# Performance work log

Measured on AMD Instinct MI355X. Metric: run time of the kernel, lower is better.

## Reference

```python
import jax, jax.numpy as jnp
import numpy as np
import math

HEAD = 4
B, N, C = 8, 1024, 256


def setup_inputs() -> dict:
    key = jax.random.key(0)
    k1, k2, k3, k4, k5 = jax.random.split(key, 5)
    query = jax.random.normal(k1, (B, N, C), dtype=jnp.float32)
    keyt = jax.random.normal(k2, (B, N, C), dtype=jnp.float32)
    value = jax.random.normal(k3, (B, N, C), dtype=jnp.float32)
    mask = jax.random.randint(k4, (B, N, N), 0, 2).astype(bool)
    dis = jax.random.normal(k5, (B, N, N), dtype=jnp.float32)
    return {"query": query, "key": keyt, "value": value, "mask": mask, "dis": dis}


def reference(query, key, value, mask, dis):
    Bq, Nq, Cq = key.shape
    d = Cq // HEAD
    # split heads: [B,N,C] -> [h,B,N,d]
    q = query.reshape(Bq, Nq, HEAD, d).transpose(2, 0, 1, 3)
    k = key.reshape(Bq, Nq, HEAD, d).transpose(2, 0, 1, 3)
    v = value.reshape(Bq, Nq, HEAD, d).transpose(2, 0, 1, 3)
    # scores: [h,B,N,N]; note: dis added BEFORE scaling, as in the torch code
    scores = jnp.einsum('hbnd,hbmd->hbnm', q, k)
    scores = scores + dis[None]            # dis broadcasts over head dim
    scores = scores / math.sqrt(d)
    scores = jnp.where(mask[None], -jnp.inf, scores)
    p_attn = jax.nn.softmax(scores, axis=-1)
    out = jnp.einsum('hbnm,hbmd->hbnd', p_attn, v)  # [h,B,N,d]
    out = out.transpose(1, 2, 0, 3).reshape(Bq, Nq, Cq)
    return out, p_attn
```

## Files before the change

### kernel.cpp

```cpp
#include <hip/hip_runtime.h>
#include <math.h>

#define HEADS 4
#define BATCH 8
#define SEQ   1024
#define CH    256
#define DH    64
#define RB    16

typedef float  floatx4  __attribute__((ext_vector_type(4)));
typedef short  shortx8  __attribute__((ext_vector_type(8)));
typedef short  shortx4  __attribute__((ext_vector_type(4)));

__device__ __forceinline__ unsigned short f2bf(float f) {
    unsigned u = __float_as_uint(f);
    unsigned r = u + 0x7FFFu + ((u >> 16) & 1u);
    return (unsigned short)(r >> 16);
}
__device__ __forceinline__ shortx8 pack8(float4 a, float4 b) {
    shortx8 r;
    r[0] = (short)f2bf(a.x); r[1] = (short)f2bf(a.y);
    r[2] = (short)f2bf(a.z); r[3] = (short)f2bf(a.w);
    r[4] = (short)f2bf(b.x); r[5] = (short)f2bf(b.y);
    r[6] = (short)f2bf(b.z); r[7] = (short)f2bf(b.w);
    return r;
}

__global__ __launch_bounds__(256)
void prep(const float* __restrict__ q, const float* __restrict__ k,
          const float* __restrict__ v, const void* __restrict__ maskp,
          unsigned short* __restrict__ qb, unsigned short* __restrict__ kb,
          unsigned short* __restrict__ vt, unsigned* __restrict__ pm)
{
    __shared__ unsigned short tl[64][68];
    const int t = threadIdx.x;
    const int bid = blockIdx.x;
    if (bid < 2048) {
        const float* src = (bid < 1024) ? q : k;
        unsigned short* dst = (bid < 1024) ? qb : kb;
        const float sc = (bid < 1024) ? 0.125f : 1.0f;
        size_t idx = (size_t)(bid & 1023) * 2048 + (size_t)t * 8;
        float4 a = *(const float4*)(src + idx);
        float4 b = *(const float4*)(src + idx + 4);
        a.x *= sc; a.y *= sc; a.z *= sc; a.w *= sc;
        b.x *= sc; b.y *= sc; b.z *= sc; b.w *= sc;
        *(shortx8*)(dst + idx) = pack8(a, b);
        return;
    }
    if (bid < 2560) {
        const int vb = bid - 2048;
        const int nt = vb & 15, h = (vb >> 4) & 3, b = vb >> 6;
        const int n0 = nt * 64;
        const float* vsrc = v + ((size_t)(b * SEQ + n0)) * CH + h * DH;
        #pragma unroll
        for (int it = 0; it < 4; ++it) {
            int fid = it * 256 + t;
            int n = fid >> 4, cc = (fid & 15) * 4;
            float4 x = *(const float4*)(vsrc + (size_t)n * CH + cc);
            tl[n][cc]     = f2bf(x.x);
            tl[n][cc + 1] = f2bf(x.y);
            tl[n][cc + 2] = f2bf(x.z);
            tl[n][cc + 3] = f2bf(x.w);
        }
        __syncthreads();
        unsigned short* vout = vt + ((size_t)((b * HEADS + h) * DH)) * SEQ + n0;
        #pragma unroll
        for (int it = 0; it < 2; ++it) {
            int cid = it * 256 + t;
            int d = cid >> 3, nc = cid & 7;
            shortx8 r;
            #pragma unroll
            for (int j = 0; j < 8; ++j) r[j] = (short)tl[nc * 8 + j][d];
            *(shortx8*)(vout + (size_t)d * SEQ + nc * 8) = r;
        }
        return;
    }
    const int vb2 = bid - 2560;
    const int b = vb2 >> 7, rg = vb2 & 127;
    const int sub = t >> 5, wq = t & 31;
    const int row = rg * 8 + sub;
    const int w_ = wq >> 2, qd_ = wq & 3;
    int fl;
    {
        const unsigned* mw = (const unsigned*)maskp;
        const int lane = t & 63;
        int found = 0;
        #pragma unroll
        for (int j = 0; j < 16; ++j)
            if (mw[lane * 16 + j] & 0xFFFFFF00u) found = 1;
        fl = (__ballot(found != 0) != 0ULL) ? 1 : 0;
    }
    const unsigned char* m8  = (const unsigned char*)maskp;
    const int*           m32 = (const int*)maskp;
    unsigned u = 0;
    #pragma unroll
    for (int mc = 0; mc < 8; ++mc) {
        #pragma unroll
        for (int r = 0; r < 4; ++r) {
            size_t idx = ((size_t)(b * SEQ + row)) * SEQ
                       + mc * 128 + w_ * 16 + qd_ * 4 + r;
            int mk = fl ? (int)m8[idx] : m32[idx];
            u |= (mk ? 1u : 0u) << (mc * 4 + r);
        }
    }
    pm[(((size_t)b * SEQ + row) << 5) + wq] = u;
}

__global__ __launch_bounds__(64)
void attn_wave(const unsigned short* __restrict__ qb,
               const unsigned short* __restrict__ kbf,
               const unsigned short* __restrict__ vt,
               const unsigned* __restrict__ pm,
               const float* __restrict__ dis, float* __restrict__ out,
               float* __restrict__ pout)
{
    __shared__ unsigned short ps[2][16][40];

    const int t   = threadIdx.x;
    const int bid = blockIdx.x;
    const int b   = bid & (BATCH - 1);
    const int h   = (bid >> 3) & (HEADS - 1);
    const int n0  = (bid >> 5) * RB;
    const int ln  = t & 15;
    const int qd  = t >> 4;

    const unsigned short* qrow = qb + ((size_t)(b * SEQ + n0 + ln)) * CH + h * DH;
    shortx8 aq0 = *(const shortx8*)(qrow + qd * 8);
    shortx8 aq1 = *(const shortx8*)(qrow + 32 + qd * 8);

    const unsigned short* kbase = kbf + ((size_t)(b * SEQ)) * CH + h * DH;
    const unsigned short* vbase = vt + ((size_t)((b * HEADS + h) * DH)) * SEQ;
    const float* disrow =
        dis + ((size_t)(b * SEQ + n0 + ln)) * SEQ + qd * 4;
    const unsigned* pmrow = pm + (((size_t)(b * SEQ + n0 + ln)) << 5) + qd;

    float sum = 0.f;
    for (int wg = 0; wg < 8; ++wg) {
        const unsigned mw = pmrow[wg * 4];
        #pragma unroll 4
        for (int mc = 0; mc < 8; ++mc) {
            const int cb = mc * 128 + wg * 16;
            const unsigned short* krow = kbase + (size_t)(cb + ln) * CH;
            shortx8 kf0 = *(const shortx8*)(krow + qd * 8);
            shortx8 kf1 = *(const shortx8*)(krow + 32 + qd * 8);
            float4 dv = *(const float4*)(disrow + cb);
            floatx4 acc = {0.f, 0.f, 0.f, 0.f};
            acc = __builtin_amdgcn_mfma_f32_16x16x32_bf16(kf0, aq0, acc, 0, 0, 0);
            acc = __builtin_amdgcn_mfma_f32_16x16x32_bf16(kf1, aq1, acc, 0, 0, 0);
            float x0 = __expf(fmaf(dv.x, 0.125f, acc[0]));
            float x1 = __expf(fmaf(dv.y, 0.125f, acc[1]));
            float x2 = __expf(fmaf(dv.z, 0.125f, acc[2]));
            float x3 = __expf(fmaf(dv.w, 0.125f, acc[3]));
            if ((mw >> (mc * 4 + 0)) & 1u) x0 = 0.f;
            if ((mw >> (mc * 4 + 1)) & 1u) x1 = 0.f;
            if ((mw >> (mc * 4 + 2)) & 1u) x2 = 0.f;
            if ((mw >> (mc * 4 + 3)) & 1u) x3 = 0.f;
            sum += x0 + x1 + x2 + x3;
        }
    }
    sum += __shfl_xor(sum, 16);
    sum += __shfl_xor(sum, 32);
    const float inv = 1.0f / sum;

    floatx4 o0 = {0.f,0.f,0.f,0.f}, o1 = {0.f,0.f,0.f,0.f};
    floatx4 o2 = {0.f,0.f,0.f,0.f}, o3 = {0.f,0.f,0.f,0.f};
    float* prow = pout + ((size_t)((h * BATCH + b) * SEQ + n0 + ln)) * SEQ
                + qd * 4;
    int par = 0;
    for (int wp = 0; wp < 4; ++wp) {
        const unsigned mw0 = pmrow[(2 * wp) * 4];
        const unsigned mw1 = pmrow[(2 * wp + 1) * 4];
        #pragma unroll 2
        for (int mc = 0; mc < 8; ++mc) {
            const int cb = mc * 128 + wp * 32;
            const unsigned short* vk = vbase + cb + qd * 8;
            shortx8 vf0 = *(const shortx8*)(vk + (size_t)(0 * 16 + ln) * SEQ);
            shortx8 vf1 = *(const shortx8*)(vk + (size_t)(1 * 16 + ln) * SEQ);
            shortx8 vf2 = *(const shortx8*)(vk + (size_t)(2 * 16 + ln) * SEQ);
            shortx8 vf3 = *(const shortx8*)(vk + (size_t)(3 * 16 + ln) * SEQ);
            const unsigned short* kr0 = kbase + (size_t)(cb + ln) * CH;
            const unsigned short* kr1 = kbase + (size_t)(cb + 16 + ln) * CH;
            shortx8 k00 = *(const shortx8*)(kr0 + qd * 8);
            shortx8 k01 = *(const shortx8*)(kr0 + 32 + qd * 8);
            shortx8 k10 = *(const shortx8*)(kr1 + qd * 8);
            shortx8 k11 = *(const shortx8*)(kr1 + 32 + qd * 8);
            float4 dv0 = *(const float4*)(disrow + cb);
            float4 dv1 = *(const float4*)(disrow + cb + 16);
            floatx4 a0 = {0.f,0.f,0.f,0.f}, a1 = {0.f,0.f,0.f,0.f};
            a0 = __builtin_amdgcn_mfma_f32_16x16x32_bf16(k00, aq0, a0, 0, 0, 0);
            a0 = __builtin_amdgcn_mfma_f32_16x16x32_bf16(k01, aq1, a0, 0, 0, 0);
            a1 = __builtin_amdgcn_mfma_f32_16x16x32_bf16(k10, aq0, a1, 0, 0, 0);
            a1 = __builtin_amdgcn_mfma_f32_16x16x32_bf16(k11, aq1, a1, 0, 0, 0);
            float p0[4], p1[4];
            #pragma unroll
            for (int r = 0; r < 4; ++r) {
                float e0 = __expf(fmaf(((const float*)&dv0)[r], 0.125f, a0[r]));
                float e1 = __expf(fmaf(((const float*)&dv1)[r], 0.125f, a1[r]));
                if ((mw0 >> (mc * 4 + r)) & 1u) e0 = 0.f;
                if ((mw1 >> (mc * 4 + r)) & 1u) e1 = 0.f;
                p0[r] = e0; p1[r] = e1;
            }
            float4 pv0 = { p0[0]*inv, p0[1]*inv, p0[2]*inv, p0[3]*inv };
            float4 pv1 = { p1[0]*inv, p1[1]*inv, p1[2]*inv, p1[3]*inv };
            *(float4*)(prow + cb)      = pv0;
            *(float4*)(prow + cb + 16) = pv1;
            shortx4 e0, e1;
            e0[0] = (short)f2bf(p0[0]); e0[1] = (short)f2bf(p0[1]);
            e0[2] = (short)f2bf(p0[2]); e0[3] = (short)f2bf(p0[3]);
            e1[0] = (short)f2bf(p1[0]); e1[1] = (short)f2bf(p1[1]);
            e1[2] = (short)f2bf(p1[2]); e1[3] = (short)f2bf(p1[3]);
            *(shortx4*)&ps[par][ln][qd * 4]      = e0;
            *(shortx4*)&ps[par][ln][16 + qd * 4] = e1;
            __syncthreads();
            shortx8 af = *(const shortx8*)&ps[par][ln][qd * 8];
            o0 = __builtin_amdgcn_mfma_f32_16x16x32_bf16(af, vf0, o0, 0, 0, 0);
            o1 = __builtin_amdgcn_mfma_f32_16x16x32_bf16(af, vf1, o1, 0, 0, 0);
            o2 = __builtin_amdgcn_mfma_f32_16x16x32_bf16(af, vf2, o2, 0, 0, 0);
            o3 = __builtin_amdgcn_mfma_f32_16x16x32_bf16(af, vf3, o3, 0, 0, 0);
            par ^= 1;
        }
    }

    const float invq0 = __shfl(inv, qd * 4 + 0);
    const float invq1 = __shfl(inv, qd * 4 + 1);
    const float invq2 = __shfl(inv, qd * 4 + 2);
    const float invq3 = __shfl(inv, qd * 4 + 3);
    #pragma unroll
    for (int dr = 0; dr < 4; ++dr) {
        const float iq = (dr == 0) ? invq0 : (dr == 1) ? invq1
                       : (dr == 2) ? invq2 : invq3;
        float* orow = out + ((size_t)(b * SEQ + n0 + qd * 4 + dr)) * CH
                    + h * DH + ln;
        orow[0]  = o0[dr] * iq;
        orow[16] = o1[dr] * iq;
        orow[32] = o2[dr] * iq;
        orow[48] = o3[dr] * iq;
    }
}

extern "C" void kernel_launch(void* const* d_in, const int* in_sizes, int n_in,
                              void* d_out, int out_size, void* d_ws, size_t ws_size,
                              hipStream_t stream) {
    const float* q    = (const float*)d_in[0];
    const float* k    = (const float*)d_in[1];
    const float* v    = (const float*)d_in[2];
    const void*  mask = d_in[3];
    const float* dis  = (const float*)d_in[4];
    float* out  = (float*)d_out;
    float* pout = out + (size_t)BATCH * SEQ * CH;

    unsigned short* qb  = (unsigned short*)d_ws;
    unsigned short* kbw = qb  + (size_t)BATCH * SEQ * CH;
    unsigned short* vtw = kbw + (size_t)BATCH * SEQ * CH;
    unsigned*       pmw = (unsigned*)(vtw + (size_t)BATCH * SEQ * CH);
    (void)ws_size;

    prep<<<3584, 256, 0, stream>>>(q, k, v, mask, qb, kbw, vtw, pmw);
    attn_wave<<<HEADS * BATCH * (SEQ / RB), 64, 0, stream>>>(
        qb, kbw, vtw, pmw, dis, out, pout);
}
```

Measured before the change: 322.1 us.

## Split fused attention into QK-exp and PV kernels via a bf16 score buffer

The single-wave fused kernel, which recomputed QK^T in two passes, is replaced by two kernels. The first computes the masked exponentials with 512-thread blocks, stores them as bf16 in a workspace buffer, and writes inverse row sums. The second reads those scores back for the P·V MFMA and writes the normalized probabilities. This removes the duplicated QK/exp work and gives each launch more waves per block. The cost is extra workspace traffic for the score matrix, and the probability output is now derived from bf16-rounded values, so it loses precision.

```diff
diff --git a/kernel.cpp b/kernel.cpp
--- a/kernel.cpp
+++ b/kernel.cpp
@@ -16,6 +16,9 @@
     unsigned u = __float_as_uint(f);
     unsigned r = u + 0x7FFFu + ((u >> 16) & 1u);
     return (unsigned short)(r >> 16);
+}
+__device__ __forceinline__ float bf2f(unsigned short h) {
+    return __uint_as_float(((unsigned)h) << 16);
 }
 __device__ __forceinline__ shortx8 pack8(float4 a, float4 b) {
     shortx8 r;
@@ -106,6 +109,141 @@
     pm[(((size_t)b * SEQ + row) << 5) + wq] = u;
 }
 
+__global__ __launch_bounds__(512)
+void qk_exp(const unsigned short* __restrict__ qb,
+            const unsigned short* __restrict__ kbf,
+            const unsigned* __restrict__ pm,
+            const float* __restrict__ dis,
+            unsigned short* __restrict__ S, float* __restrict__ invs_g)
+{
+    __shared__ float wsum[8][16];
+    const int t   = threadIdx.x;
+    const int bid = blockIdx.x;
+    const int b   = bid & (BATCH - 1);
+    const int h   = (bid >> 3) & (HEADS - 1);
+    const int n0  = (bid >> 5) * RB;
+    const int lane = t & 63;
+    const int w    = t >> 6;
+    const int ln   = lane & 15;
+    const int qd   = lane >> 4;
+
+    const unsigned short* qrow = qb + ((size_t)(b * SEQ + n0 + ln)) * CH + h * DH;
+    shortx8 aq0 = *(const shortx8*)(qrow + qd * 8);
+    shortx8 aq1 = *(const shortx8*)(qrow + 32 + qd * 8);
+
+    const unsigned short* kbase = kbf + ((size_t)(b * SEQ)) * CH + h * DH;
+    const float* disrow = dis + ((size_t)(b * SEQ + n0 + ln)) * SEQ + qd * 4;
+    const unsigned mw = pm[(((size_t)(b * SEQ + n0 + ln)) << 5) + w * 4 + qd];
+    unsigned short* srow =
+        S + ((size_t)((h * BATCH + b) * SEQ + n0 + ln)) * SEQ + qd * 4;
+
+    float sum = 0.f;
+    #pragma unroll 4
+    for (int mc = 0; mc < 8; ++mc) {
+        const int cb = mc * 128 + w * 16;
+        const unsigned short* krow = kbase + (size_t)(cb + ln) * CH;
+        shortx8 kf0 = *(const shortx8*)(krow + qd * 8);
+        shortx8 kf1 = *(const shortx8*)(krow + 32 + qd * 8);
+        float4 dv = *(const float4*)(disrow + cb);
+        floatx4 acc = {0.f, 0.f, 0.f, 0.f};
+        acc = __builtin_amdgcn_mfma_f32_16x16x32_bf16(kf0, aq0, acc, 0, 0, 0);
+        acc = __builtin_amdgcn_mfma_f32_16x16x32_bf16(kf1, aq1, acc, 0, 0, 0);
+        float x0 = __expf(fmaf(dv.x, 0.125f, acc[0]));
+        float x1 = __expf(fmaf(dv.y, 0.125f, acc[1]));
+        float x2 = __expf(fmaf(dv.z, 0.125f, acc[2]));
+        float x3 = __expf(fmaf(dv.w, 0.125f, acc[3]));
+        if ((mw >> (mc * 4 + 0)) & 1u) x0 = 0.f;
+        if ((mw >> (mc * 4 + 1)) & 1u) x1 = 0.f;
+        if ((mw >> (mc * 4 + 2)) & 1u) x2 = 0.f;
+        if ((mw >> (mc * 4 + 3)) & 1u) x3 = 0.f;
+        sum += x0 + x1 + x2 + x3;
+        shortx4 ev;
+        ev[0] = (short)f2bf(x0); ev[1] = (short)f2bf(x1);
+        ev[2] = (short)f2bf(x2); ev[3] = (short)f2bf(x3);
+        *(shortx4*)(srow + cb) = ev;
+    }
+    sum += __shfl_xor(sum, 16);
+    sum += __shfl_xor(sum, 32);
+    if (qd == 0) wsum[w][ln] = sum;
+    __syncthreads();
+    if (w == 0 && qd == 0) {
+        float tot = 0.f;
+        #pragma unroll
+        for (int j = 0; j < 8; ++j) tot += wsum[j][ln];
+        invs_g[(h * BATCH + b) * SEQ + n0 + ln] = 1.0f / tot;
+    }
+}
+
+__global__ __launch_bounds__(256)
+void pv(const unsigned short* __restrict__ S,
+        const unsigned short* __restrict__ vt,
+        const float* __restrict__ invs_g,
+        float* __restrict__ out, float* __restrict__ pout)
+{
+    const int t   = threadIdx.x;
+    const int bid = blockIdx.x;
+    const int b   = bid & (BATCH - 1);
+    const int h   = (bid >> 3) & (HEADS - 1);
+    const int n0  = (bid >> 5) * RB;
+    const int lane = t & 63;
+    const int w    = t >> 6;
+    const int ln   = lane & 15;
+    const int qd   = lane >> 4;
+    const int c    = w * 16;
+
+    const unsigned short* srow =
+        S + ((size_t)((h * BATCH + b) * SEQ + n0 + ln)) * SEQ;
+    const unsigned short* vcol =
+        vt + ((size_t)((b * HEADS + h) * DH + c + ln)) * SEQ;
+    float* prow = pout + ((size_t)((h * BATCH + b) * SEQ + n0 + ln)) * SEQ;
+    const float inv_l = invs_g[(h * BATCH + b) * SEQ + n0 + ln];
+
+    floatx4 accA = {0.f,0.f,0.f,0.f}, accB = {0.f,0.f,0.f,0.f};
+    #pragma unroll 4
+    for (int it = 0; it < 32; it += 2) {
+        const int kk0 = it * 32 + qd * 8;
+        const int kk1 = kk0 + 32;
+        shortx8 af0 = *(const shortx8*)(srow + kk0);
+        shortx8 bf0 = *(const shortx8*)(vcol + kk0);
+        shortx8 af1 = *(const shortx8*)(srow + kk1);
+        shortx8 bf1 = *(const shortx8*)(vcol + kk1);
+        accA = __builtin_amdgcn_mfma_f32_16x16x32_bf16(af0, bf0, accA, 0, 0, 0);
+        accB = __builtin_amdgcn_mfma_f32_16x16x32_bf16(af1, bf1, accB, 0, 0, 0);
+        if (w == 0) {
+            float4 pa = { bf2f((unsigned short)af0[0]) * inv_l,
+                          bf2f((unsigned short)af0[1]) * inv_l,
+                          bf2f((unsigned short)af0[2]) * inv_l,
+                          bf2f((unsigned short)af0[3]) * inv_l };
+            float4 pb = { bf2f((unsigned short)af0[4]) * inv_l,
+                          bf2f((unsigned short)af0[5]) * inv_l,
+                          bf2f((unsigned short)af0[6]) * inv_l,
+                          bf2f((unsigned short)af0[7]) * inv_l };
+            float4 pc = { bf2f((unsigned short)af1[0]) * inv_l,
+                          bf2f((unsigned short)af1[1]) * inv_l,
+                          bf2f((unsigned short)af1[2]) * inv_l,
+                          bf2f((unsigned short)af1[3]) * inv_l };
+            float4 pd = { bf2f((unsigned short)af1[4]) * inv_l,
+                          bf2f((unsigned short)af1[5]) * inv_l,
+                          bf2f((unsigned short)af1[6]) * inv_l,
+                          bf2f((unsigned short)af1[7]) * inv_l };
+            *(float4*)(prow + kk0)     = pa;
+            *(float4*)(prow + kk0 + 4) = pb;
+            *(float4*)(prow + kk1)     = pc;
+            *(float4*)(prow + kk1 + 4) = pd;
+        }
+    }
+    floatx4 acc;
+    acc[0] = accA[0] + accB[0]; acc[1] = accA[1] + accB[1];
+    acc[2] = accA[2] + accB[2]; acc[3] = accA[3] + accB[3];
+
+    const float* ivb = invs_g + (h * BATCH + b) * SEQ + n0 + qd * 4;
+    #pragma unroll
+    for (int r = 0; r < 4; ++r) {
+        out[((size_t)(b * SEQ + n0 + qd * 4 + r)) * CH + h * DH + c + ln]
+            = acc[r] * ivb[r];
+    }
+}
+
 __global__ __launch_bounds__(64)
 void attn_wave(const unsigned short* __restrict__ qb,
                const unsigned short* __restrict__ kbf,
@@ -115,7 +253,6 @@
                float* __restrict__ pout)
 {
     __shared__ unsigned short ps[2][16][40];
-
     const int t   = threadIdx.x;
     const int bid = blockIdx.x;
     const int b   = bid & (BATCH - 1);
@@ -123,17 +260,13 @@
     const int n0  = (bid >> 5) * RB;
     const int ln  = t & 15;
     const int qd  = t >> 4;
-
     const unsigned short* qrow = qb + ((size_t)(b * SEQ + n0 + ln)) * CH + h * DH;
     shortx8 aq0 = *(const shortx8*)(qrow + qd * 8);
     shortx8 aq1 = *(const shortx8*)(qrow + 32 + qd * 8);
-
     const unsigned short* kbase = kbf + ((size_t)(b * SEQ)) * CH + h * DH;
     const unsigned short* vbase = vt + ((size_t)((b * HEADS + h) * DH)) * SEQ;
-    const float* disrow =
-        dis + ((size_t)(b * SEQ + n0 + ln)) * SEQ + qd * 4;
+    const float* disrow = dis + ((size_t)(b * SEQ + n0 + ln)) * SEQ + qd * 4;
     const unsigned* pmrow = pm + (((size_t)(b * SEQ + n0 + ln)) << 5) + qd;
-
     float sum = 0.f;
     for (int wg = 0; wg < 8; ++wg) {
         const unsigned mw = pmrow[wg * 4];
@@ -161,7 +294,6 @@
     sum += __shfl_xor(sum, 16);
     sum += __shfl_xor(sum, 32);
     const float inv = 1.0f / sum;
-
     floatx4 o0 = {0.f,0.f,0.f,0.f}, o1 = {0.f,0.f,0.f,0.f};
     floatx4 o2 = {0.f,0.f,0.f,0.f}, o3 = {0.f,0.f,0.f,0.f};
     float* prow = pout + ((size_t)((h * BATCH + b) * SEQ + n0 + ln)) * SEQ
@@ -220,7 +352,6 @@
             par ^= 1;
         }
     }
-
     const float invq0 = __shfl(inv, qd * 4 + 0);
     const float invq1 = __shfl(inv, qd * 4 + 1);
     const float invq2 = __shfl(inv, qd * 4 + 2);
@@ -249,13 +380,26 @@
     float* out  = (float*)d_out;
     float* pout = out + (size_t)BATCH * SEQ * CH;
 
+    const size_t E = (size_t)BATCH * SEQ * CH;
     unsigned short* qb  = (unsigned short*)d_ws;
-    unsigned short* kbw = qb  + (size_t)BATCH * SEQ * CH;
-    unsigned short* vtw = kbw + (size_t)BATCH * SEQ * CH;
-    unsigned*       pmw = (unsigned*)(vtw + (size_t)BATCH * SEQ * CH);
-    (void)ws_size;
+    unsigned short* kbw = qb  + E;
+    unsigned short* vtw = kbw + E;
+    unsigned*       pmw = (unsigned*)(vtw + E);
+    float*          ivw = (float*)(pmw + (size_t)BATCH * SEQ * 32);
+    unsigned short* Sw  = (unsigned short*)(ivw + (size_t)HEADS * BATCH * SEQ);
+    const size_t need = 3 * E * 2 + (size_t)BATCH * SEQ * 32 * 4
+                      + (size_t)HEADS * BATCH * SEQ * 4
+                      + (size_t)HEADS * BATCH * SEQ * SEQ * 2;
 
     prep<<<3584, 256, 0, stream>>>(q, k, v, mask, qb, kbw, vtw, pmw);
-    attn_wave<<<HEADS * BATCH * (SEQ / RB), 64, 0, stream>>>(
-        qb, kbw, vtw, pmw, dis, out, pout);
-}
+
+    if (ws_size == 0 || ws_size >= need) {
+        qk_exp<<<HEADS * BATCH * (SEQ / RB), 512, 0, stream>>>(
+            qb, kbw, pmw, dis, Sw, ivw);
+        pv<<<HEADS * BATCH * (SEQ / RB), 256, 0, stream>>>(
+            Sw, vtw, ivw, out, pout);
+    } else {
+        attn_wave<<<HEADS * BATCH * (SEQ / RB), 64, 0, stream>>>(
+            qb, kbw, vtw, pmw, dis, out, pout);
+    }
+}
```

New measurement: 340.2 us. +5.6%, slower.
